# Kernel optimization log

Hardware: AMD Instinct MI355X
Metric: run time of the kernel (lower is better)

Reference implementation:

```python
import jax, jax.numpy as jnp
import numpy as np

B, T, D = 64, 4096, 256
UNITS = 256  # must equal D due to the module's build() wiring


def setup_inputs() -> dict:
    key = jax.random.key(0)
    k1, k2, k3 = jax.random.split(key, 3)
    inputs = jax.random.normal(k1, (B, T, D), dtype=jnp.float32)
    # Glorot-uniform-ish init for Dense kernels, zeros for biases (Keras defaults)
    lim_w = np.sqrt(6.0 / (D + UNITS)).astype(np.float32)
    W_w = jax.random.uniform(k2, (D, UNITS), jnp.float32, -lim_w, lim_w)
    W_b = jnp.zeros((UNITS,), jnp.float32)
    lim_v = np.sqrt(6.0 / (UNITS + 1)).astype(np.float32)
    V_w = jax.random.uniform(k3, (UNITS, 1), jnp.float32, -lim_v, lim_v)
    V_b = jnp.zeros((1,), jnp.float32)
    return {"inputs": inputs, "W_w": W_w, "W_b": W_b, "V_w": V_w, "V_b": V_b}


def reference(inputs, W_w, W_b, V_w, V_b):
    # score: [B, T, UNITS]
    score = jnp.tanh(jnp.einsum('btd,du->btu', inputs, W_w) + W_b)
    # logits: [B, T, 1]; softmax over time axis (axis=1)
    logits = jnp.einsum('btu,uo->bto', score, V_w) + V_b
    attn = jax.nn.softmax(logits, axis=1)  # [B, T, 1]
    # weighted sum over time -> [B, D]
    context = jnp.sum(attn * inputs, axis=1)
    return context
```

## Files before the change

### kernel.cpp

```cpp
#include <hip/hip_runtime.h>
#include <hip/hip_bf16.h>
#include <math.h>

#define BB 64
#define TT 4096
#define DD 256
#define UU 256
#define MT 64
#define NT (TT/MT)
#define LDA 264

typedef __attribute__((ext_vector_type(8))) short bf16x8;
typedef __attribute__((ext_vector_type(4))) float f32x4;

static __device__ __forceinline__ short f2bf(float f){
  unsigned u = __float_as_uint(f);
  u = (u + 0x7fffu + ((u >> 16) & 1u)) >> 16;
  return (short)u;
}

static __device__ __forceinline__ unsigned pk_bf16(float a, float b){
#if __has_builtin(__builtin_amdgcn_cvt_pk_bf16_f32)
  typedef __bf16 bf16v2 __attribute__((ext_vector_type(2)));
  bf16v2 r = __builtin_amdgcn_cvt_pk_bf16_f32(a, b);
  unsigned u; __builtin_memcpy(&u, &r, 4); return u;
#else
  unsigned ua = __float_as_uint(a), ub = __float_as_uint(b);
  ua = (ua + 0x7fffu + ((ua >> 16) & 1u)) >> 16;
  ub = (ub + 0x7fffu + ((ub >> 16) & 1u)) & 0xffff0000u;
  return ub | ua;
#endif
}

__global__ void wfrag_kernel(const float* __restrict__ W, short* __restrict__ Wf){
  int g  = blockIdx.x*256 + threadIdx.x;
  int l  = g & 63;
  int f  = g >> 6;
  int kt = f & 7, nf = (f >> 3) & 3, wv = f >> 5;
  int lo = l & 15, quad = l >> 4;
  int u  = wv*64 + nf*16 + lo;
  int d0 = kt*32 + quad*8;
  bf16x8 v;
  #pragma unroll
  for (int j=0;j<8;++j) v[j] = f2bf(W[(size_t)(d0+j)*UU + u]);
  *reinterpret_cast<bf16x8*>(&Wf[(size_t)g*8]) = v;
}

__global__ __launch_bounds__(256)
void attn_tile_kernel(const float* __restrict__ X, const short* __restrict__ Wf,
                      const float* __restrict__ Wb, const float* __restrict__ Vw,
                      float* __restrict__ m_part, float* __restrict__ l_part,
                      float* __restrict__ ctx_part)
{
  __shared__ short a_tile[MT*LDA];
  __shared__ float s_part[4][MT];
  __shared__ float s_pw[4][MT];
  __shared__ float s_red[8][264];

  const int tid  = threadIdx.x;
  const int lane = tid & 63;
  const int wv   = tid >> 6;
  const int lo   = lane & 15;
  const int quad = lane >> 4;
  const int u_base = wv*64 + lo;
  const int b  = blockIdx.x >> 6;
  const int tt = blockIdx.x & 63;
  const size_t xbase = ((size_t)b*TT + (size_t)tt*MT)*DD;
  const int rgrp  = tid >> 5;
  const int cbase = (tid & 31)*8;

  float wb_r[4], v_r[4];
  #pragma unroll
  for (int nf=0; nf<4; ++nf){
    wb_r[nf] = Wb[u_base + nf*16];
    v_r[nf]  = Vw[u_base + nf*16];
  }
  const short* wf_base = Wf + ((size_t)(wv*32*64 + lane))*8;

  float4 pf[16];
  #pragma unroll
  for (int p8=0; p8<8; ++p8){
    const float4* src = reinterpret_cast<const float4*>(
        X + xbase + (size_t)(p8*8 + rgrp)*DD + cbase);
    pf[2*p8]   = src[0];
    pf[2*p8+1] = src[1];
  }

  #pragma unroll
  for (int p8=0; p8<8; ++p8){
    int4 v;
    v.x = (int)pk_bf16(pf[2*p8].x,   pf[2*p8].y);
    v.y = (int)pk_bf16(pf[2*p8].z,   pf[2*p8].w);
    v.z = (int)pk_bf16(pf[2*p8+1].x, pf[2*p8+1].y);
    v.w = (int)pk_bf16(pf[2*p8+1].z, pf[2*p8+1].w);
    *reinterpret_cast<int4*>(&a_tile[(p8*8 + rgrp)*LDA + cbase]) = v;
  }
  __syncthreads();

  f32x4 acc[4][4];
  #pragma unroll
  for (int mf=0; mf<4; ++mf)
    #pragma unroll
    for (int nf=0; nf<4; ++nf)
      acc[mf][nf] = (f32x4){0.f,0.f,0.f,0.f};

  #pragma unroll
  for (int kt=0; kt<8; ++kt){
    const int k0 = kt*32 + quad*8;
    bf16x8 af[4];
    #pragma unroll
    for (int mf=0; mf<4; ++mf)
      af[mf] = *reinterpret_cast<const bf16x8*>(&a_tile[(mf*16 + lo)*LDA + k0]);
    #pragma unroll
    for (int nf=0; nf<4; ++nf){
      bf16x8 bfv = *reinterpret_cast<const bf16x8*>(wf_base + (nf*8 + kt)*512);
      #pragma unroll
      for (int mf=0; mf<4; ++mf)
        acc[mf][nf] = __builtin_amdgcn_mfma_f32_16x16x32_bf16(af[mf], bfv, acc[mf][nf], 0, 0, 0);
    }
  }

  #pragma unroll
  for (int mf=0; mf<4; ++mf){
    #pragma unroll
    for (int r=0; r<4; ++r){
      float part = 0.f;
      #pragma unroll
      for (int nf=0; nf<4; ++nf){
        float s  = acc[mf][nf][r] + wb_r[nf];
        float e2 = __expf(2.f*s);
        float th = 1.f - 2.f/(e2 + 1.f);
        part = fmaf(th, v_r[nf], part);
      }
      part += __shfl_xor(part, 1);
      part += __shfl_xor(part, 2);
      part += __shfl_xor(part, 4);
      part += __shfl_xor(part, 8);
      if (lo == 0) s_part[wv][mf*16 + quad*4 + r] = part;
    }
  }
  __syncthreads();

  float lt = s_part[0][lane] + s_part[1][lane] + s_part[2][lane] + s_part[3][lane];
  float mx = lt;
  #pragma unroll
  for (int o=32; o; o>>=1) mx = fmaxf(mx, __shfl_xor(mx, o));
  float p = __expf(lt - mx);
  float sum = p;
  #pragma unroll
  for (int o=32; o; o>>=1) sum += __shfl_xor(sum, o);
  s_pw[wv][lane] = p;

  float cp[8] = {0.f,0.f,0.f,0.f,0.f,0.f,0.f,0.f};
  #pragma unroll
  for (int p8=0; p8<8; ++p8){
    float pr = s_pw[wv][p8*8 + rgrp];
    cp[0] = fmaf(pr, pf[2*p8].x,   cp[0]);
    cp[1] = fmaf(pr, pf[2*p8].y,   cp[1]);
    cp[2] = fmaf(pr, pf[2*p8].z,   cp[2]);
    cp[3] = fmaf(pr, pf[2*p8].w,   cp[3]);
    cp[4] = fmaf(pr, pf[2*p8+1].x, cp[4]);
    cp[5] = fmaf(pr, pf[2*p8+1].y, cp[5]);
    cp[6] = fmaf(pr, pf[2*p8+1].z, cp[6]);
    cp[7] = fmaf(pr, pf[2*p8+1].w, cp[7]);
  }
  *reinterpret_cast<float4*>(&s_red[rgrp][cbase])   = (float4){cp[0],cp[1],cp[2],cp[3]};
  *reinterpret_cast<float4*>(&s_red[rgrp][cbase+4]) = (float4){cp[4],cp[5],cp[6],cp[7]};
  __syncthreads();

  float ctx = 0.f;
  #pragma unroll
  for (int g=0; g<8; ++g) ctx += s_red[g][tid];

  if (tid == 0){ m_part[blockIdx.x] = mx; l_part[blockIdx.x] = sum; }
  ctx_part[(size_t)blockIdx.x*DD + tid] = ctx;
}

__global__ void merge_kernel(const float* __restrict__ m_part, const float* __restrict__ l_part,
                             const float* __restrict__ ctx_part, float* __restrict__ out)
{
  int b = blockIdx.x;
  int d = threadIdx.x;
  float mg = -INFINITY;
  #pragma unroll 8
  for (int i=0; i<NT; ++i) mg = fmaxf(mg, m_part[b*NT+i]);
  float lg = 0.f, s = 0.f;
  #pragma unroll 8
  for (int i=0; i<NT; ++i){
    float w = __expf(m_part[b*NT+i] - mg);
    lg += l_part[b*NT+i] * w;
    s  += ctx_part[(size_t)(b*NT+i)*DD + d] * w;
  }
  out[b*DD + d] = s / lg;
}

extern "C" void kernel_launch(void* const* d_in, const int* in_sizes, int n_in,
                              void* d_out, int out_size, void* d_ws, size_t ws_size,
                              hipStream_t stream)
{
  const float* X  = (const float*)d_in[0];
  const float* Ww = (const float*)d_in[1];
  const float* Wb = (const float*)d_in[2];
  const float* Vw = (const float*)d_in[3];
  float* out = (float*)d_out;

  short* Wf       = (short*)d_ws;
  float* m_part   = (float*)((char*)d_ws + (size_t)UU*DD*sizeof(short));
  float* l_part   = m_part + BB*NT;
  float* ctx_part = l_part + BB*NT;

  wfrag_kernel<<<32, 256, 0, stream>>>(Ww, Wf);
  attn_tile_kernel<<<BB*NT, 256, 0, stream>>>(X, Wf, Wb, Vw, m_part, l_part, ctx_part);
  merge_kernel<<<BB, DD, 0, stream>>>(m_part, l_part, ctx_part, out);
}
```

Measured before the change: 429.7 us.

## Halve time tile, drop fp32 register prefetch, and parallelize merge across groups

Reduces the per-block time tile from 64 to 32 rows and sets launch bounds for higher occupancy. The fp32 copy of X is no longer held in registers; the weighted context sum reads the bf16 tile from LDS instead. The merge kernel uses 1024 threads, splitting partial tiles across four groups with a shared-memory reduction. This aims to cut register pressure and improve latency hiding on the bandwidth-bound tile kernel, at the cost of doubled partial outputs and a bf16-precision context sum.

```diff
diff --git a/kernel.cpp b/kernel.cpp
--- a/kernel.cpp
+++ b/kernel.cpp
@@ -6,7 +6,7 @@
 #define TT 4096
 #define DD 256
 #define UU 256
-#define MT 64
+#define MT 32
 #define NT (TT/MT)
 #define LDA 264
 
@@ -46,7 +46,7 @@
   *reinterpret_cast<bf16x8*>(&Wf[(size_t)g*8]) = v;
 }
 
-__global__ __launch_bounds__(256)
+__global__ __launch_bounds__(256, 5)
 void attn_tile_kernel(const float* __restrict__ X, const short* __restrict__ Wf,
                       const float* __restrict__ Wb, const float* __restrict__ Vw,
                       float* __restrict__ m_part, float* __restrict__ l_part,
@@ -63,8 +63,8 @@
   const int lo   = lane & 15;
   const int quad = lane >> 4;
   const int u_base = wv*64 + lo;
-  const int b  = blockIdx.x >> 6;
-  const int tt = blockIdx.x & 63;
+  const int b  = blockIdx.x >> 7;
+  const int tt = blockIdx.x & 127;
   const size_t xbase = ((size_t)b*TT + (size_t)tt*MT)*DD;
   const int rgrp  = tid >> 5;
   const int cbase = (tid & 31)*8;
@@ -77,29 +77,24 @@
   }
   const short* wf_base = Wf + ((size_t)(wv*32*64 + lane))*8;
 
-  float4 pf[16];
-  #pragma unroll
-  for (int p8=0; p8<8; ++p8){
+  #pragma unroll
+  for (int p8=0; p8<4; ++p8){
     const float4* src = reinterpret_cast<const float4*>(
         X + xbase + (size_t)(p8*8 + rgrp)*DD + cbase);
-    pf[2*p8]   = src[0];
-    pf[2*p8+1] = src[1];
-  }
-
-  #pragma unroll
-  for (int p8=0; p8<8; ++p8){
+    float4 x0 = src[0];
+    float4 x1 = src[1];
     int4 v;
-    v.x = (int)pk_bf16(pf[2*p8].x,   pf[2*p8].y);
-    v.y = (int)pk_bf16(pf[2*p8].z,   pf[2*p8].w);
-    v.z = (int)pk_bf16(pf[2*p8+1].x, pf[2*p8+1].y);
-    v.w = (int)pk_bf16(pf[2*p8+1].z, pf[2*p8+1].w);
+    v.x = (int)pk_bf16(x0.x, x0.y);
+    v.y = (int)pk_bf16(x0.z, x0.w);
+    v.z = (int)pk_bf16(x1.x, x1.y);
+    v.w = (int)pk_bf16(x1.z, x1.w);
     *reinterpret_cast<int4*>(&a_tile[(p8*8 + rgrp)*LDA + cbase]) = v;
   }
   __syncthreads();
 
-  f32x4 acc[4][4];
-  #pragma unroll
-  for (int mf=0; mf<4; ++mf)
+  f32x4 acc[2][4];
+  #pragma unroll
+  for (int mf=0; mf<2; ++mf)
     #pragma unroll
     for (int nf=0; nf<4; ++nf)
       acc[mf][nf] = (f32x4){0.f,0.f,0.f,0.f};
@@ -107,21 +102,21 @@
   #pragma unroll
   for (int kt=0; kt<8; ++kt){
     const int k0 = kt*32 + quad*8;
-    bf16x8 af[4];
-    #pragma unroll
-    for (int mf=0; mf<4; ++mf)
+    bf16x8 af[2];
+    #pragma unroll
+    for (int mf=0; mf<2; ++mf)
       af[mf] = *reinterpret_cast<const bf16x8*>(&a_tile[(mf*16 + lo)*LDA + k0]);
     #pragma unroll
     for (int nf=0; nf<4; ++nf){
       bf16x8 bfv = *reinterpret_cast<const bf16x8*>(wf_base + (nf*8 + kt)*512);
       #pragma unroll
-      for (int mf=0; mf<4; ++mf)
+      for (int mf=0; mf<2; ++mf)
         acc[mf][nf] = __builtin_amdgcn_mfma_f32_16x16x32_bf16(af[mf], bfv, acc[mf][nf], 0, 0, 0);
     }
   }
 
   #pragma unroll
-  for (int mf=0; mf<4; ++mf){
+  for (int mf=0; mf<2; ++mf){
     #pragma unroll
     for (int r=0; r<4; ++r){
       float part = 0.f;
@@ -141,28 +136,27 @@
   }
   __syncthreads();
 
-  float lt = s_part[0][lane] + s_part[1][lane] + s_part[2][lane] + s_part[3][lane];
+  const int li = lane & 31;
+  float lt = s_part[0][li] + s_part[1][li] + s_part[2][li] + s_part[3][li];
   float mx = lt;
   #pragma unroll
-  for (int o=32; o; o>>=1) mx = fmaxf(mx, __shfl_xor(mx, o));
+  for (int o=16; o; o>>=1) mx = fmaxf(mx, __shfl_xor(mx, o));
   float p = __expf(lt - mx);
   float sum = p;
   #pragma unroll
-  for (int o=32; o; o>>=1) sum += __shfl_xor(sum, o);
-  s_pw[wv][lane] = p;
+  for (int o=16; o; o>>=1) sum += __shfl_xor(sum, o);
+  s_pw[wv][li] = p;
 
   float cp[8] = {0.f,0.f,0.f,0.f,0.f,0.f,0.f,0.f};
   #pragma unroll
-  for (int p8=0; p8<8; ++p8){
+  for (int p8=0; p8<4; ++p8){
     float pr = s_pw[wv][p8*8 + rgrp];
-    cp[0] = fmaf(pr, pf[2*p8].x,   cp[0]);
-    cp[1] = fmaf(pr, pf[2*p8].y,   cp[1]);
-    cp[2] = fmaf(pr, pf[2*p8].z,   cp[2]);
-    cp[3] = fmaf(pr, pf[2*p8].w,   cp[3]);
-    cp[4] = fmaf(pr, pf[2*p8+1].x, cp[4]);
-    cp[5] = fmaf(pr, pf[2*p8+1].y, cp[5]);
-    cp[6] = fmaf(pr, pf[2*p8+1].z, cp[6]);
-    cp[7] = fmaf(pr, pf[2*p8+1].w, cp[7]);
+    bf16x8 xv = *reinterpret_cast<const bf16x8*>(&a_tile[(p8*8 + rgrp)*LDA + cbase]);
+    #pragma unroll
+    for (int j=0; j<8; ++j){
+      float x = __uint_as_float(((unsigned)(unsigned short)xv[j]) << 16);
+      cp[j] = fmaf(pr, x, cp[j]);
+    }
   }
   *reinterpret_cast<float4*>(&s_red[rgrp][cbase])   = (float4){cp[0],cp[1],cp[2],cp[3]};
   *reinterpret_cast<float4*>(&s_red[rgrp][cbase+4]) = (float4){cp[4],cp[5],cp[6],cp[7]};
@@ -176,22 +170,36 @@
   ctx_part[(size_t)blockIdx.x*DD + tid] = ctx;
 }
 
-__global__ void merge_kernel(const float* __restrict__ m_part, const float* __restrict__ l_part,
-                             const float* __restrict__ ctx_part, float* __restrict__ out)
+__global__ __launch_bounds__(1024)
+void merge_kernel(const float* __restrict__ m_part, const float* __restrict__ l_part,
+                  const float* __restrict__ ctx_part, float* __restrict__ out)
 {
-  int b = blockIdx.x;
-  int d = threadIdx.x;
+  __shared__ float s_sum[4][256];
+  const int b = blockIdx.x;
+  const int g = threadIdx.x >> 8;
+  const int d = threadIdx.x & 255;
+
   float mg = -INFINITY;
+  #pragma unroll 16
+  for (int i=0; i<NT; ++i) mg = fmaxf(mg, m_part[b*NT+i]);
+  float lg = 0.f;
+  #pragma unroll 16
+  for (int i=0; i<NT; ++i) lg += l_part[b*NT+i] * __expf(m_part[b*NT+i] - mg);
+
+  float s = 0.f;
   #pragma unroll 8
-  for (int i=0; i<NT; ++i) mg = fmaxf(mg, m_part[b*NT+i]);
-  float lg = 0.f, s = 0.f;
-  #pragma unroll 8
-  for (int i=0; i<NT; ++i){
-    float w = __expf(m_part[b*NT+i] - mg);
-    lg += l_part[b*NT+i] * w;
-    s  += ctx_part[(size_t)(b*NT+i)*DD + d] * w;
-  }
-  out[b*DD + d] = s / lg;
+  for (int i=0; i<32; ++i){
+    int t = g*32 + i;
+    float w = __expf(m_part[b*NT+t] - mg);
+    s = fmaf(w, ctx_part[(size_t)(b*NT+t)*DD + d], s);
+  }
+  s_sum[g][d] = s;
+  __syncthreads();
+  if (threadIdx.x < 256){
+    float tot = s_sum[0][threadIdx.x] + s_sum[1][threadIdx.x]
+              + s_sum[2][threadIdx.x] + s_sum[3][threadIdx.x];
+    out[b*DD + threadIdx.x] = tot / lg;
+  }
 }
 
 extern "C" void kernel_launch(void* const* d_in, const int* in_sizes, int n_in,
@@ -211,5 +219,5 @@
 
   wfrag_kernel<<<32, 256, 0, stream>>>(Ww, Wf);
   attn_tile_kernel<<<BB*NT, 256, 0, stream>>>(X, Wf, Wb, Vw, m_part, l_part, ctx_part);
-  merge_kernel<<<BB, DD, 0, stream>>>(m_part, l_part, ctx_part, out);
-}
+  merge_kernel<<<BB, 1024, 0, stream>>>(m_part, l_part, ctx_part, out);
+}
```

Measured after the change: 420.4 us. -2.2%, faster.
